# Kernel tuning notes

Hardware: AMD Instinct MI355X
Metric: run time of the kernel (lower is better)

## Reference

```python
import jax, jax.numpy as jnp
import numpy as np

MIN_NORM = 1e-15
EPS = 1e-5
C_CURV = 1.0  # args.c

def _norm(x):
    return jnp.clip(jnp.linalg.norm(x, axis=-1, keepdims=True), MIN_NORM)

def artanh(x):
    x = jnp.clip(x, -1.0 + EPS, 1.0 - EPS)
    return 0.5 * (jnp.log1p(x) - jnp.log1p(-x))

def proj(x, c):
    # clip points to stay strictly inside the Poincare ball
    norm = _norm(x)
    maxnorm = (1.0 - EPS) / jnp.sqrt(c)
    return jnp.where(norm > maxnorm, x / norm * maxnorm, x)

def expmap0(u, c):
    sqrt_c = jnp.sqrt(c)
    u_norm = _norm(u)
    return jnp.tanh(sqrt_c * u_norm) * u / (sqrt_c * u_norm)

def logmap0(p, c):
    sqrt_c = jnp.sqrt(c)
    p_norm = _norm(p)
    return artanh(sqrt_c * p_norm) * p / (sqrt_c * p_norm)

def mobius_add(x, y, c):
    x2 = jnp.sum(x * x, axis=-1, keepdims=True)
    y2 = jnp.sum(y * y, axis=-1, keepdims=True)
    xy = jnp.sum(x * y, axis=-1, keepdims=True)
    num = (1.0 + 2.0 * c * xy + c * y2) * x + (1.0 - c * x2) * y
    denom = 1.0 + 2.0 * c * xy + c * c * x2 * y2
    return num / jnp.clip(denom, MIN_NORM)

def mobius_matvec(W, x, c):
    sqrt_c = jnp.sqrt(c)
    x_norm = _norm(x)
    mx = x @ W.T
    mx_norm = _norm(mx)
    return jnp.tanh(mx_norm / x_norm * artanh(sqrt_c * x_norm)) * mx / (mx_norm * sqrt_c)

def poincare_dist(x, y, c):
    sqrt_c = jnp.sqrt(c)
    d = _norm(mobius_add(-x, y, c))[..., 0]
    return 2.0 / sqrt_c * artanh(sqrt_c * d)

def hgnn_layer(h, adj, W, b, c):
    # HypLinear: mobius matvec + hyperbolic bias
    mv = proj(mobius_matvec(W, h, c), c)
    hyp_b = proj(expmap0(b, c), c)
    h = proj(mobius_add(mv, hyp_b, c), c)
    # HypAgg: aggregate in tangent space at origin
    h = proj(expmap0(adj @ logmap0(h, c), c), c)
    # HypAct: relu in tangent space
    return proj(expmap0(jax.nn.relu(logmap0(h, c)), c), c)

def setup_inputs() -> dict:
    key = jax.random.key(0)
    ks = jax.random.split(key, 10)
    N, D, C, NC, NODE_C, L = 8192, 128, 64, 7, 7, 4
    x = jax.random.normal(ks[0], (N, D), jnp.float32)
    adj = jax.random.uniform(ks[1], (N, N), jnp.float32) / N  # row-stochastic-ish dense adjacency
    graph_indicator = jax.random.randint(ks[2], (N,), 0, 1)
    W_conv = jax.random.normal(ks[3], (L, D, D), jnp.float32) / np.sqrt(D)
    b_conv = jax.random.normal(ks[4], (L, D), jnp.float32) * 0.01
    centroids = jax.random.normal(ks[5], (C, D), jnp.float32) * 0.1
    W_mlp = jax.random.normal(ks[6], (NC, C), jnp.float32) * 0.1
    b_mlp = jnp.zeros((NC,), jnp.float32)
    W_mlp1 = jax.random.normal(ks[7], (NODE_C, D), jnp.float32) * 0.1
    b_mlp1 = jnp.zeros((NODE_C,), jnp.float32)
    return {"x": x, "adj": adj, "graph_indicator": graph_indicator,
            "W_conv": W_conv, "b_conv": b_conv, "centroids": centroids,
            "W_mlp": W_mlp, "b_mlp": b_mlp, "W_mlp1": W_mlp1, "b_mlp1": b_mlp1}

def reference(x, adj, graph_indicator, W_conv, b_conv, centroids, W_mlp, b_mlp, W_mlp1, b_mlp1):
    c = C_CURV
    # proj_tan0 is identity for PoincareBall
    h = proj(expmap0(x, c), c)
    # 2 residual blocks, each with 2 HGNN layers; shortcut is identity (in_dim == out_dim)
    for blk in range(2):
        res = h
        for j in range(2):
            idx = blk * 2 + j
            h = hgnn_layer(h, adj, W_conv[idx], b_conv[idx], c)
        h = h + res  # Euclidean residual, as in the source
    # CentroidDistance: pairwise hyperbolic distance [N, C]
    node_centroid_dist = poincare_dist(h[:, None, :], centroids[None, :, :], c)
    readout = jnp.mean(node_centroid_dist, axis=0, keepdims=True)  # [1, C]
    h_r = logmap0(readout, c)  # proj_tan0(logmap0(.)) -> identity proj_tan0
    logits = jax.nn.softmax(h_r @ W_mlp.T + b_mlp, axis=0)[None]        # [1,1,NC]
    h1 = logmap0(h, c)
    logits_node = jax.nn.softmax(h1 @ W_mlp1.T + b_mlp1, axis=0)[None]  # [1,N,node_classes]
    return (logits, logits_node, h_r)
```

## Files before the change

### kernel.cpp

```cpp
#include <hip/hip_runtime.h>

#define MIN_NORM 1e-15f
#define EPSV 1e-5f
#define MAXN (1.0f - EPSV)
#define NN 8192
#define DD 128

typedef unsigned short u16;
typedef __bf16 bf16x8 __attribute__((ext_vector_type(8)));
typedef float f32x4 __attribute__((ext_vector_type(4)));

__device__ __forceinline__ float wave_sum(float v) {
#pragma unroll
  for (int off = 32; off > 0; off >>= 1) v += __shfl_xor(v, off, 64);
  return v;
}

__device__ __forceinline__ float artanh_f(float x) {
  x = fminf(fmaxf(x, -1.0f + EPSV), 1.0f - EPSV);
  return 0.5f * (log1pf(x) - log1pf(-x));
}

__device__ __forceinline__ u16 f2bf(float f) {
  unsigned u = __float_as_uint(f);
  unsigned r = (u + 0x7fffu + ((u >> 16) & 1u)) >> 16;
  return (u16)r;
}
__device__ __forceinline__ float bf2f(u16 b) { return __uint_as_float(((unsigned)b) << 16); }

__device__ __forceinline__ void gload16(const u16* g, u16* l) {
  __builtin_amdgcn_global_load_lds((const __attribute__((address_space(1))) void*)(g),
                                   (__attribute__((address_space(3))) void*)(l), 16, 0, 0);
}

template <bool TILED>
__global__ __launch_bounds__(256) void gemm_bt(const u16* __restrict__ A,
                                               const u16* __restrict__ Bt,
                                               float* __restrict__ Cp,
                                               int M, int K, int KC) {
  __shared__ __align__(16) u16 Ash[3 * 64 * 64];
  __shared__ __align__(16) u16 Bsh[3 * 128 * 64];

  const int tid = threadIdx.x;
  const int lane = tid & 63;
  const int w = tid >> 6;
  const int wm = w >> 1, wn = w & 1;
  const int lrow = lane & 15;
  const int lq = lane >> 4;
  const int m0 = blockIdx.x * 64;
  const int kk0 = blockIdx.y * KC;
  const int kt0 = kk0 >> 6;
  const int bxK = blockIdx.x * (K >> 6);

  const int srow = lane >> 3;
  const int spc = lane & 7;

  const u16* Ap = A + (TILED ? 0 : (size_t)m0 * K);

  f32x4 acc[2][4];
#pragma unroll
  for (int a = 0; a < 2; a++)
#pragma unroll
    for (int b = 0; b < 4; b++)
#pragma unroll
      for (int r = 0; r < 4; r++) acc[a][b][r] = 0.0f;

#define STAGE(bf, tkt, kk)                                                     \
  do {                                                                         \
    if constexpr (TILED) {                                                     \
      const u16* at = A + (((size_t)(bxK + (tkt))) << 12) + (lane << 3);       \
      _Pragma("unroll") for (int ii = 0; ii < 2; ii++)                         \
        gload16(at + ((ii * 4 + w) << 9), &Ash[(bf) * 4096 + ((ii * 4 + w) << 9)]); \
      const u16* bt2 = Bt + (((size_t)(tkt)) << 13) + (lane << 3);             \
      _Pragma("unroll") for (int ii = 0; ii < 4; ii++)                         \
        gload16(bt2 + ((ii * 4 + w) << 9), &Bsh[(bf) * 8192 + ((ii * 4 + w) << 9)]); \
    } else {                                                                   \
      _Pragma("unroll") for (int ii = 0; ii < 2; ii++) {                       \
        int rw = ((ii * 4 + w) << 3) + srow;                                   \
        gload16(Ap + (size_t)rw * K + (kk) + ((spc ^ (rw & 7)) << 3),          \
                &Ash[(bf) * 4096 + ((ii * 4 + w) << 9)]);                      \
      }                                                                        \
      _Pragma("unroll") for (int ii = 0; ii < 4; ii++) {                       \
        int rw = ((ii * 4 + w) << 3) + srow;                                   \
        gload16(Bt + (size_t)rw * K + (kk) + ((spc ^ (rw & 7)) << 3),          \
                &Bsh[(bf) * 8192 + ((ii * 4 + w) << 9)]);                      \
      }                                                                        \
    }                                                                          \
  } while (0)

#define COMPUTE(bf)                                                            \
  do {                                                                         \
    const int abase = (bf) * 4096, bbase = (bf) * 8192;                        \
    _Pragma("unroll") for (int ks = 0; ks < 2; ks++) {                         \
      const int lc = ks * 4 + lq;                                              \
      bf16x8 af[2], bfr[4];                                                    \
      _Pragma("unroll") for (int ti = 0; ti < 2; ti++) {                       \
        int r = wm * 32 + ti * 16 + lrow;                                      \
        af[ti] = *(const bf16x8*)&Ash[abase + r * 64 + ((lc ^ (r & 7)) << 3)]; \
      }                                                                        \
      _Pragma("unroll") for (int tj = 0; tj < 4; tj++) {                       \
        int n = wn * 64 + tj * 16 + lrow;                                      \
        bfr[tj] = *(const bf16x8*)&Bsh[bbase + n * 64 + ((lc ^ (n & 7)) << 3)]; \
      }                                                                        \
      _Pragma("unroll") for (int ti = 0; ti < 2; ti++)                         \
        _Pragma("unroll") for (int tj = 0; tj < 4; tj++)                       \
          acc[ti][tj] = __builtin_amdgcn_mfma_f32_16x16x32_bf16(af[ti], bfr[tj], acc[ti][tj], 0, 0, 0); \
    }                                                                          \
  } while (0)

  const int nt = KC >> 6;
  STAGE(0, kt0, kk0);
  if (nt > 1) STAGE(1, kt0 + 1, kk0 + 64);

  for (int t = 0; t < nt - 1; t++) {
    asm volatile("s_waitcnt vmcnt(6)" ::: "memory");
    __builtin_amdgcn_s_barrier();
    if (t + 2 < nt) {
      const int b2 = (t + 2) % 3;
      STAGE(b2, kt0 + t + 2, kk0 + (t + 2) * 64);
    }
    COMPUTE(t % 3);
  }
  asm volatile("s_waitcnt vmcnt(0)" ::: "memory");
  __builtin_amdgcn_s_barrier();
  COMPUTE((nt - 1) % 3);
#undef STAGE
#undef COMPUTE

  float* C = Cp + (size_t)blockIdx.y * M * 128;
#pragma unroll
  for (int ti = 0; ti < 2; ti++)
#pragma unroll
    for (int tj = 0; tj < 4; tj++)
#pragma unroll
      for (int r = 0; r < 4; r++) {
        int row = m0 + wm * 32 + ti * 16 + lq * 4 + r;
        int col = wn * 64 + tj * 16 + lrow;
        C[(size_t)row * 128 + col] = acc[ti][tj][r];
      }
}

__global__ __launch_bounds__(256) void cvt_tile(const float* __restrict__ src,
                                                u16* __restrict__ dst) {
  int tid = threadIdx.x;
  int xb = blockIdx.x;
  int kg = blockIdx.y;
  int ch = tid & 63;
  int rs = tid >> 6;
#pragma unroll
  for (int rr = 0; rr < 16; rr++) {
    int row = rr * 4 + rs;
    int gk = kg * 512 + ch * 8;
    const float* s = src + (size_t)(xb * 64 + row) * NN + gk;
    float4 a = *(const float4*)s;
    float4 b = *(const float4*)(s + 4);
    ushort4 d0, d1;
    d0.x = f2bf(a.x); d0.y = f2bf(a.y); d0.z = f2bf(a.z); d0.w = f2bf(a.w);
    d1.x = f2bf(b.x); d1.y = f2bf(b.y); d1.z = f2bf(b.z); d1.w = f2bf(b.w);
    u16* d = dst + (((size_t)(xb * 128 + (gk >> 6))) << 12) + row * 64 +
             ((((gk >> 3) & 7) ^ (row & 7)) << 3);
    *(ushort4*)d = d0;
    *(ushort4*)(d + 4) = d1;
  }
}

__global__ void build_wt(const float* __restrict__ W, u16* __restrict__ Wt2) {
  int idx = blockIdx.x * 256 + threadIdx.x;
  if (idx >= 4 * 128 * 128) return;
  int layer = idx >> 14;
  int n = (idx >> 7) & 127;
  int k = idx & 127;
  float e = W[idx];
  u16 hi = f2bf(e);
  u16 lo = f2bf(e - bf2f(hi));
  u16* base = Wt2 + (size_t)layer * 128 * 384 + (size_t)n * 384;
  base[k] = hi;
  base[128 + k] = hi;
  base[256 + k] = lo;
}

__device__ __forceinline__ void write_split(u16* hs, int i, int lane, float v0, float v1) {
  u16* row = hs + (size_t)i * 384;
  u16 h0 = f2bf(v0), h1 = f2bf(v1);
  u16 l0 = f2bf(v0 - bf2f(h0)), l1 = f2bf(v1 - bf2f(h1));
  row[lane] = h0;         row[lane + 64] = h1;
  row[128 + lane] = l0;   row[128 + 64 + lane] = l1;
  row[256 + lane] = h0;   row[256 + 64 + lane] = h1;
}

__global__ __launch_bounds__(64) void rowwise_init(const float* __restrict__ x,
                                                   float* __restrict__ h,
                                                   float* __restrict__ res,
                                                   u16* __restrict__ hsplit) {
  int i = blockIdx.x, lane = threadIdx.x;
  const float* xr = x + (size_t)i * DD;
  float a0 = xr[lane], a1 = xr[lane + 64];
  float n = fmaxf(sqrtf(wave_sum(a0 * a0 + a1 * a1)), MIN_NORM);
  float g = tanhf(n) / n;
  float y0 = g * a0, y1 = g * a1;
  float pn = fmaxf(sqrtf(wave_sum(y0 * y0 + y1 * y1)), MIN_NORM);
  float s = pn > MAXN ? MAXN / pn : 1.0f;
  y0 *= s; y1 *= s;
  size_t base = (size_t)i * DD;
  h[base + lane] = y0;   h[base + lane + 64] = y1;
  res[base + lane] = y0; res[base + lane + 64] = y1;
  write_split(hsplit, i, lane, y0, y1);
}

__global__ __launch_bounds__(64) void rowwise_mid(const float* __restrict__ h,
                                                  const float* __restrict__ P,
                                                  const float* __restrict__ bvec,
                                                  u16* __restrict__ uT2) {
  int i = blockIdx.x, lane = threadIdx.x;
  size_t base = (size_t)i * DD;
  const float* hr = h + base;
  float h0 = hr[lane], h1 = hr[lane + 64];
  float m0 = 0.f, m1 = 0.f;
#pragma unroll
  for (int sk = 0; sk < 3; sk++) {
    const float* p = P + (size_t)sk * NN * DD + base;
    m0 += p[lane];
    m1 += p[lane + 64];
  }
  float xn = fmaxf(sqrtf(wave_sum(h0 * h0 + h1 * h1)), MIN_NORM);
  float mn = fmaxf(sqrtf(wave_sum(m0 * m0 + m1 * m1)), MIN_NORM);
  float t = tanhf(mn / xn * artanh_f(xn));
  float v0 = t * m0 / mn, v1 = t * m1 / mn;
  float pn = fmaxf(sqrtf(wave_sum(v0 * v0 + v1 * v1)), MIN_NORM);
  float sc = pn > MAXN ? MAXN / pn : 1.0f;
  v0 *= sc; v1 *= sc;
  float b0 = bvec[lane], b1 = bvec[lane + 64];
  float bn = fmaxf(sqrtf(wave_sum(b0 * b0 + b1 * b1)), MIN_NORM);
  float gb = tanhf(bn) / bn;
  float e0 = gb * b0, e1 = gb * b1;
  float en = fmaxf(sqrtf(wave_sum(e0 * e0 + e1 * e1)), MIN_NORM);
  float sb = en > MAXN ? MAXN / en : 1.0f;
  e0 *= sb; e1 *= sb;
  float x2 = wave_sum(v0 * v0 + v1 * v1);
  float y2 = wave_sum(e0 * e0 + e1 * e1);
  float xy = wave_sum(v0 * e0 + v1 * e1);
  float ca = 1.0f + 2.0f * xy + y2;
  float cb = 1.0f - x2;
  float den = fmaxf(1.0f + 2.0f * xy + x2 * y2, MIN_NORM);
  float t0 = (ca * v0 + cb * e0) / den, t1 = (ca * v1 + cb * e1) / den;
  float tn = fmaxf(sqrtf(wave_sum(t0 * t0 + t1 * t1)), MIN_NORM);
  float st = tn > MAXN ? MAXN / tn : 1.0f;
  t0 *= st; t1 *= st;
  float pn2 = fmaxf(sqrtf(wave_sum(t0 * t0 + t1 * t1)), MIN_NORM);
  float gl = artanh_f(pn2) / pn2;
  u16* tb = uT2 + (((size_t)(i >> 6)) << 13);
  int c8 = (i >> 3) & 7, k7 = i & 7;
  tb[lane * 64 + (((c8) ^ (lane & 7)) << 3) + k7] = f2bf(gl * t0);
  int n2 = lane + 64;
  tb[n2 * 64 + (((c8) ^ (n2 & 7)) << 3) + k7] = f2bf(gl * t1);
}

__global__ __launch_bounds__(64) void rowwise_post(const float* __restrict__ P,
                                                   float* __restrict__ h,
                                                   float* __restrict__ res,
                                                   u16* __restrict__ hsplit,
                                                   int addres) {
  int i = blockIdx.x, lane = threadIdx.x;
  size_t base = (size_t)i * DD;
  float m0 = 0.f, m1 = 0.f;
#pragma unroll
  for (int sk = 0; sk < 8; sk++) {
    const float* p = P + (size_t)sk * NN * DD + base;
    m0 += p[lane];
    m1 += p[lane + 64];
  }
  float n = fmaxf(sqrtf(wave_sum(m0 * m0 + m1 * m1)), MIN_NORM);
  float g = tanhf(n) / n;
  float y0 = g * m0, y1 = g * m1;
  float pn = fmaxf(sqrtf(wave_sum(y0 * y0 + y1 * y1)), MIN_NORM);
  float s = pn > MAXN ? MAXN / pn : 1.0f;
  y0 *= s; y1 *= s;
  float hn = fmaxf(sqrtf(wave_sum(y0 * y0 + y1 * y1)), MIN_NORM);
  float gl = artanh_f(hn) / hn;
  float u0 = fmaxf(gl * y0, 0.0f), u1 = fmaxf(gl * y1, 0.0f);
  float un = fmaxf(sqrtf(wave_sum(u0 * u0 + u1 * u1)), MIN_NORM);
  float ge = tanhf(un) / un;
  float z0 = ge * u0, z1 = ge * u1;
  float zn = fmaxf(sqrtf(wave_sum(z0 * z0 + z1 * z1)), MIN_NORM);
  float sz = zn > MAXN ? MAXN / zn : 1.0f;
  z0 *= sz; z1 *= sz;
  if (addres) {
    z0 += res[base + lane];
    z1 += res[base + lane + 64];
    res[base + lane] = z0;
    res[base + lane + 64] = z1;
  }
  h[base + lane] = z0;
  h[base + lane + 64] = z1;
  write_split(hsplit, i, lane, z0, z1);
}

__global__ __launch_bounds__(256) void centroid_k(const float* __restrict__ h,
                                                  const float* __restrict__ cen,
                                                  float* __restrict__ rs) {
  __shared__ float cs[64 * 129];
  __shared__ float hs[32 * 128];
  __shared__ float y2s[64];
  int tid = threadIdx.x;
  int i0 = blockIdx.x * 32;
  for (int idx = tid; idx < 64 * 128; idx += 256) {
    int r = idx >> 7, c = idx & 127;
    cs[r * 129 + c] = cen[idx];
  }
  for (int idx = tid; idx < 32 * 128; idx += 256) hs[idx] = h[(size_t)i0 * 128 + idx];
  __syncthreads();
  if (tid < 64) {
    float s = 0.f;
    for (int k = 0; k < 128; k++) { float v = cs[tid * 129 + k]; s = fmaf(v, v, s); }
    y2s[tid] = s;
  }
  __syncthreads();
  int w = tid >> 6, lane = tid & 63;
  float dsum = 0.f;
  for (int rr = 0; rr < 8; rr++) {
    int r = w * 8 + rr;
    float dot = 0.f, x2 = 0.f;
    for (int k = 0; k < 128; k++) {
      float hk = hs[r * 128 + k];
      dot = fmaf(hk, cs[lane * 129 + k], dot);
      x2 = fmaf(hk, hk, x2);
    }
    float y2 = y2s[lane];
    float al = 1.0f - 2.0f * dot + y2;
    float be = 1.0f - x2;
    float num2 = al * al * x2 + be * be * y2 - 2.0f * al * be * dot;
    float den = fmaxf(1.0f - 2.0f * dot + x2 * y2, MIN_NORM);
    float d = fmaxf(sqrtf(fmaxf(num2, 0.0f)) / den, MIN_NORM);
    dsum += 2.0f * artanh_f(d);
  }
  atomicAdd(&rs[lane], dsum);
}

__global__ __launch_bounds__(64) void finalize_k(const float* __restrict__ rs,
                                                 float* __restrict__ out) {
  int lane = threadIdx.x;
  float r = rs[lane] * (1.0f / 8192.0f);
  float n = fmaxf(sqrtf(wave_sum(r * r)), MIN_NORM);
  float a = artanh_f(n);
  out[7 + NN * 7 + lane] = a * r / n;
  if (lane < 7) out[lane] = 1.0f;
}

__global__ __launch_bounds__(64) void scores_k(const float* __restrict__ h,
                                               const float* __restrict__ Wm,
                                               const float* __restrict__ bm,
                                               float* __restrict__ sc) {
  int i = blockIdx.x, lane = threadIdx.x;
  const float* hr = h + (size_t)i * DD;
  float h0 = hr[lane], h1 = hr[lane + 64];
  float pn = fmaxf(sqrtf(wave_sum(h0 * h0 + h1 * h1)), MIN_NORM);
  float gl = artanh_f(pn) / pn;
  float u0 = gl * h0, u1 = gl * h1;
  float p[7];
#pragma unroll
  for (int j = 0; j < 7; j++)
    p[j] = wave_sum(u0 * Wm[j * 128 + lane] + u1 * Wm[j * 128 + lane + 64]);
  float v = p[0];
#pragma unroll
  for (int j = 1; j < 7; j++)
    if (lane == j) v = p[j];
  if (lane < 7) sc[(size_t)i * 7 + lane] = v + bm[lane];
}

__global__ __launch_bounds__(256) void softmax_col(const float* __restrict__ sc,
                                                   float* __restrict__ out) {
  __shared__ float buf[256][8];
  int tid = threadIdx.x;
  float mx[7];
#pragma unroll
  for (int j = 0; j < 7; j++) mx[j] = -1e30f;
  for (int i = tid; i < NN; i += 256)
#pragma unroll
    for (int j = 0; j < 7; j++) mx[j] = fmaxf(mx[j], sc[i * 7 + j]);
#pragma unroll
  for (int j = 0; j < 7; j++) buf[tid][j] = mx[j];
  __syncthreads();
  for (int off = 128; off > 0; off >>= 1) {
    if (tid < off)
#pragma unroll
      for (int j = 0; j < 7; j++) buf[tid][j] = fmaxf(buf[tid][j], buf[tid + off][j]);
    __syncthreads();
  }
  float cm[7];
#pragma unroll
  for (int j = 0; j < 7; j++) cm[j] = buf[0][j];
  __syncthreads();
  float sm[7];
#pragma unroll
  for (int j = 0; j < 7; j++) sm[j] = 0.f;
  for (int i = tid; i < NN; i += 256)
#pragma unroll
    for (int j = 0; j < 7; j++) sm[j] += expf(sc[i * 7 + j] - cm[j]);
#pragma unroll
  for (int j = 0; j < 7; j++) buf[tid][j] = sm[j];
  __syncthreads();
  for (int off = 128; off > 0; off >>= 1) {
    if (tid < off)
#pragma unroll
      for (int j = 0; j < 7; j++) buf[tid][j] += buf[tid + off][j];
    __syncthreads();
  }
  float csum[7];
#pragma unroll
  for (int j = 0; j < 7; j++) csum[j] = buf[0][j];
  __syncthreads();
  for (int idx = tid; idx < NN * 7; idx += 256) {
    int i = idx / 7, j = idx - i * 7;
    out[idx] = expf(sc[i * 7 + j] - cm[j]) / csum[j];
  }
}

extern "C" void kernel_launch(void* const* d_in, const int* in_sizes, int n_in,
                              void* d_out, int out_size, void* d_ws, size_t ws_size,
                              hipStream_t stream) {
  const float* x = (const float*)d_in[0];
  const float* adj = (const float*)d_in[1];
  const float* W_conv = (const float*)d_in[3];
  const float* b_conv = (const float*)d_in[4];
  const float* centroids = (const float*)d_in[5];
  const float* W_mlp1 = (const float*)d_in[8];
  const float* b_mlp1 = (const float*)d_in[9];
  float* out = (float*)d_out;

  char* ws = (char*)d_ws;
  size_t off = 0;
  auto alloc = [&](size_t bytes) {
    void* p = ws + off;
    off = (off + bytes + 255) & ~(size_t)255;
    return p;
  };
  float* h = (float*)alloc((size_t)NN * DD * 4);
  float* res = (float*)alloc((size_t)NN * DD * 4);
  u16* hsplit = (u16*)alloc((size_t)NN * 384 * 2);
  u16* uT2 = (u16*)alloc((size_t)DD * NN * 2);
  u16* Wt2 = (u16*)alloc((size_t)4 * 128 * 384 * 2);
  float* P = (float*)alloc((size_t)8 * NN * DD * 4);
  u16* adjT = (u16*)alloc((size_t)NN * NN * 2);
  float* scores = (float*)alloc((size_t)NN * 7 * 4);
  float* rs = (float*)alloc(64 * 4);
  (void)ws_size; (void)in_sizes; (void)n_in; (void)out_size;

  hipMemsetAsync(rs, 0, 64 * 4, stream);
  build_wt<<<(4 * 128 * 128 + 255) / 256, 256, 0, stream>>>(W_conv, Wt2);
  rowwise_init<<<NN, 64, 0, stream>>>(x, h, res, hsplit);
  cvt_tile<<<dim3(128, 16), 256, 0, stream>>>(adj, adjT);
  for (int layer = 0; layer < 4; layer++) {
    gemm_bt<false><<<dim3(NN / 64, 3), 256, 0, stream>>>(
        hsplit, Wt2 + (size_t)layer * 128 * 384, P, NN, 384, 128);
    rowwise_mid<<<NN, 64, 0, stream>>>(h, P, b_conv + layer * DD, uT2);
    gemm_bt<true><<<dim3(NN / 64, 8), 256, 0, stream>>>(
        adjT, uT2, P, NN, NN, NN / 8);
    rowwise_post<<<NN, 64, 0, stream>>>(P, h, res, hsplit, (layer & 1));
  }
  centroid_k<<<256, 256, 0, stream>>>(h, centroids, rs);
  finalize_k<<<1, 64, 0, stream>>>(rs, out);
  scores_k<<<NN, 64, 0, stream>>>(h, W_mlp1, b_mlp1, scores);
  softmax_col<<<1, 256, 0, stream>>>(scores, out + 7);
}
```

Measured before the change: 812.5 us.

## Fuse HypLinear epilogue into W GEMM, parallelize column softmax, halve adj split-K

Drops the split-K W GEMM plus separate rowwise_mid kernel. A single GEMM over full K now computes per-row norms and the bias dot product through shuffle and LDS reductions, then applies the Mobius/proj/logmap math in its epilogue and writes the tiled bf16 operand directly. Bias expmap/proj and the input row norms are precomputed in small kernels. The adj GEMM split-K goes from 8 to 4, which cuts partial-sum traffic but leaves fewer blocks. The single-block column softmax is replaced by atomicMax with an order-preserving encoding, a multi-block sum with atomicAdd, and a parallel write kernel.

```diff
diff --git a/kernel.cpp b/kernel.cpp
--- a/kernel.cpp
+++ b/kernel.cpp
@@ -28,16 +28,24 @@
 }
 __device__ __forceinline__ float bf2f(u16 b) { return __uint_as_float(((unsigned)b) << 16); }
 
+__device__ __forceinline__ unsigned fenc(float x) {
+  unsigned u = __float_as_uint(x);
+  return (u & 0x80000000u) ? ~u : (u | 0x80000000u);
+}
+__device__ __forceinline__ float fdec(unsigned k) {
+  unsigned u = (k & 0x80000000u) ? (k & 0x7fffffffu) : ~k;
+  return __uint_as_float(u);
+}
+
 __device__ __forceinline__ void gload16(const u16* g, u16* l) {
   __builtin_amdgcn_global_load_lds((const __attribute__((address_space(1))) void*)(g),
                                    (__attribute__((address_space(3))) void*)(l), 16, 0, 0);
 }
 
-template <bool TILED>
-__global__ __launch_bounds__(256) void gemm_bt(const u16* __restrict__ A,
-                                               const u16* __restrict__ Bt,
-                                               float* __restrict__ Cp,
-                                               int M, int K, int KC) {
+__global__ __launch_bounds__(256) void gemm_adj(const u16* __restrict__ A,
+                                                const u16* __restrict__ Bt,
+                                                float* __restrict__ Cp,
+                                                int KC) {
   __shared__ __align__(16) u16 Ash[3 * 64 * 64];
   __shared__ __align__(16) u16 Bsh[3 * 128 * 64];
 
@@ -48,14 +56,8 @@
   const int lrow = lane & 15;
   const int lq = lane >> 4;
   const int m0 = blockIdx.x * 64;
-  const int kk0 = blockIdx.y * KC;
-  const int kt0 = kk0 >> 6;
-  const int bxK = blockIdx.x * (K >> 6);
-
-  const int srow = lane >> 3;
-  const int spc = lane & 7;
-
-  const u16* Ap = A + (TILED ? 0 : (size_t)m0 * K);
+  const int kt0 = (blockIdx.y * KC) >> 6;
+  const int bxK = blockIdx.x * (NN >> 6);
 
   f32x4 acc[2][4];
 #pragma unroll
@@ -65,60 +67,43 @@
 #pragma unroll
       for (int r = 0; r < 4; r++) acc[a][b][r] = 0.0f;
 
-#define STAGE(bf, tkt, kk)                                                     \
-  do {                                                                         \
-    if constexpr (TILED) {                                                     \
-      const u16* at = A + (((size_t)(bxK + (tkt))) << 12) + (lane << 3);       \
-      _Pragma("unroll") for (int ii = 0; ii < 2; ii++)                         \
-        gload16(at + ((ii * 4 + w) << 9), &Ash[(bf) * 4096 + ((ii * 4 + w) << 9)]); \
-      const u16* bt2 = Bt + (((size_t)(tkt)) << 13) + (lane << 3);             \
-      _Pragma("unroll") for (int ii = 0; ii < 4; ii++)                         \
-        gload16(bt2 + ((ii * 4 + w) << 9), &Bsh[(bf) * 8192 + ((ii * 4 + w) << 9)]); \
-    } else {                                                                   \
-      _Pragma("unroll") for (int ii = 0; ii < 2; ii++) {                       \
-        int rw = ((ii * 4 + w) << 3) + srow;                                   \
-        gload16(Ap + (size_t)rw * K + (kk) + ((spc ^ (rw & 7)) << 3),          \
-                &Ash[(bf) * 4096 + ((ii * 4 + w) << 9)]);                      \
-      }                                                                        \
-      _Pragma("unroll") for (int ii = 0; ii < 4; ii++) {                       \
-        int rw = ((ii * 4 + w) << 3) + srow;                                   \
-        gload16(Bt + (size_t)rw * K + (kk) + ((spc ^ (rw & 7)) << 3),          \
-                &Bsh[(bf) * 8192 + ((ii * 4 + w) << 9)]);                      \
-      }                                                                        \
-    }                                                                          \
+#define STAGE(bf, tkt)                                                          \
+  do {                                                                          \
+    const u16* at = A + (((size_t)(bxK + (tkt))) << 12) + (lane << 3);          \
+    _Pragma("unroll") for (int ii = 0; ii < 2; ii++)                            \
+      gload16(at + ((ii * 4 + w) << 9), &Ash[(bf) * 4096 + ((ii * 4 + w) << 9)]); \
+    const u16* bt2 = Bt + (((size_t)(tkt)) << 13) + (lane << 3);                \
+    _Pragma("unroll") for (int ii = 0; ii < 4; ii++)                            \
+      gload16(bt2 + ((ii * 4 + w) << 9), &Bsh[(bf) * 8192 + ((ii * 4 + w) << 9)]); \
   } while (0)
 
-#define COMPUTE(bf)                                                            \
-  do {                                                                         \
-    const int abase = (bf) * 4096, bbase = (bf) * 8192;                        \
-    _Pragma("unroll") for (int ks = 0; ks < 2; ks++) {                         \
-      const int lc = ks * 4 + lq;                                              \
-      bf16x8 af[2], bfr[4];                                                    \
-      _Pragma("unroll") for (int ti = 0; ti < 2; ti++) {                       \
-        int r = wm * 32 + ti * 16 + lrow;                                      \
-        af[ti] = *(const bf16x8*)&Ash[abase + r * 64 + ((lc ^ (r & 7)) << 3)]; \
-      }                                                                        \
-      _Pragma("unroll") for (int tj = 0; tj < 4; tj++) {                       \
-        int n = wn * 64 + tj * 16 + lrow;                                      \
+#define COMPUTE(bf)                                                             \
+  do {                                                                          \
+    const int abase = (bf) * 4096, bbase = (bf) * 8192;                         \
+    _Pragma("unroll") for (int ks = 0; ks < 2; ks++) {                          \
+      const int lc = ks * 4 + lq;                                               \
+      bf16x8 af[2], bfr[4];                                                     \
+      _Pragma("unroll") for (int ti = 0; ti < 2; ti++) {                        \
+        int r = wm * 32 + ti * 16 + lrow;                                       \
+        af[ti] = *(const bf16x8*)&Ash[abase + r * 64 + ((lc ^ (r & 7)) << 3)];  \
+      }                                                                         \
+      _Pragma("unroll") for (int tj = 0; tj < 4; tj++) {                        \
+        int n = wn * 64 + tj * 16 + lrow;                                       \
         bfr[tj] = *(const bf16x8*)&Bsh[bbase + n * 64 + ((lc ^ (n & 7)) << 3)]; \
-      }                                                                        \
-      _Pragma("unroll") for (int ti = 0; ti < 2; ti++)                         \
-        _Pragma("unroll") for (int tj = 0; tj < 4; tj++)                       \
+      }                                                                         \
+      _Pragma("unroll") for (int ti = 0; ti < 2; ti++)                          \
+        _Pragma("unroll") for (int tj = 0; tj < 4; tj++)                        \
           acc[ti][tj] = __builtin_amdgcn_mfma_f32_16x16x32_bf16(af[ti], bfr[tj], acc[ti][tj], 0, 0, 0); \
-    }                                                                          \
+    }                                                                           \
   } while (0)
 
   const int nt = KC >> 6;
-  STAGE(0, kt0, kk0);
-  if (nt > 1) STAGE(1, kt0 + 1, kk0 + 64);
-
+  STAGE(0, kt0);
+  STAGE(1, kt0 + 1);
   for (int t = 0; t < nt - 1; t++) {
     asm volatile("s_waitcnt vmcnt(6)" ::: "memory");
     __builtin_amdgcn_s_barrier();
-    if (t + 2 < nt) {
-      const int b2 = (t + 2) % 3;
-      STAGE(b2, kt0 + t + 2, kk0 + (t + 2) * 64);
-    }
+    if (t + 2 < nt) STAGE((t + 2) % 3, kt0 + t + 2);
     COMPUTE(t % 3);
   }
   asm volatile("s_waitcnt vmcnt(0)" ::: "memory");
@@ -127,7 +112,7 @@
 #undef STAGE
 #undef COMPUTE
 
-  float* C = Cp + (size_t)blockIdx.y * M * 128;
+  float* C = Cp + (size_t)blockIdx.y * NN * 128;
 #pragma unroll
   for (int ti = 0; ti < 2; ti++)
 #pragma unroll
@@ -138,6 +123,150 @@
         int col = wn * 64 + tj * 16 + lrow;
         C[(size_t)row * 128 + col] = acc[ti][tj][r];
       }
+}
+
+__global__ __launch_bounds__(256) void wgemm_mid(const u16* __restrict__ A,
+                                                 const u16* __restrict__ Bt,
+                                                 const float* __restrict__ hnorm,
+                                                 const float* __restrict__ eb,
+                                                 const float* __restrict__ ey2,
+                                                 u16* __restrict__ uT2) {
+  __shared__ __align__(16) u16 Ash[3 * 64 * 64];
+  __shared__ __align__(16) u16 Bsh[3 * 128 * 64];
+
+  const int tid = threadIdx.x;
+  const int lane = tid & 63;
+  const int w = tid >> 6;
+  const int wm = w >> 1, wn = w & 1;
+  const int lrow = lane & 15;
+  const int lq = lane >> 4;
+  const int m0 = blockIdx.x * 64;
+  const int srow = lane >> 3, spc = lane & 7;
+  const int K = 384;
+  const u16* Ap = A + (size_t)m0 * K;
+
+  f32x4 acc[2][4];
+#pragma unroll
+  for (int a = 0; a < 2; a++)
+#pragma unroll
+    for (int b = 0; b < 4; b++)
+#pragma unroll
+      for (int r = 0; r < 4; r++) acc[a][b][r] = 0.0f;
+
+#define STAGE(bf, kk)                                                           \
+  do {                                                                          \
+    _Pragma("unroll") for (int ii = 0; ii < 2; ii++) {                          \
+      int rw = ((ii * 4 + w) << 3) + srow;                                      \
+      gload16(Ap + (size_t)rw * K + (kk) + ((spc ^ (rw & 7)) << 3),             \
+              &Ash[(bf) * 4096 + ((ii * 4 + w) << 9)]);                         \
+    }                                                                           \
+    _Pragma("unroll") for (int ii = 0; ii < 4; ii++) {                          \
+      int rw = ((ii * 4 + w) << 3) + srow;                                      \
+      gload16(Bt + (size_t)rw * K + (kk) + ((spc ^ (rw & 7)) << 3),             \
+              &Bsh[(bf) * 8192 + ((ii * 4 + w) << 9)]);                         \
+    }                                                                           \
+  } while (0)
+
+#define COMPUTE(bf)                                                             \
+  do {                                                                          \
+    const int abase = (bf) * 4096, bbase = (bf) * 8192;                         \
+    _Pragma("unroll") for (int ks = 0; ks < 2; ks++) {                          \
+      const int lc = ks * 4 + lq;                                               \
+      bf16x8 af[2], bfr[4];                                                     \
+      _Pragma("unroll") for (int ti = 0; ti < 2; ti++) {                        \
+        int r = wm * 32 + ti * 16 + lrow;                                       \
+        af[ti] = *(const bf16x8*)&Ash[abase + r * 64 + ((lc ^ (r & 7)) << 3)];  \
+      }                                                                         \
+      _Pragma("unroll") for (int tj = 0; tj < 4; tj++) {                        \
+        int n = wn * 64 + tj * 16 + lrow;                                       \
+        bfr[tj] = *(const bf16x8*)&Bsh[bbase + n * 64 + ((lc ^ (n & 7)) << 3)]; \
+      }                                                                         \
+      _Pragma("unroll") for (int ti = 0; ti < 2; ti++)                          \
+        _Pragma("unroll") for (int tj = 0; tj < 4; tj++)                        \
+          acc[ti][tj] = __builtin_amdgcn_mfma_f32_16x16x32_bf16(af[ti], bfr[tj], acc[ti][tj], 0, 0, 0); \
+    }                                                                           \
+  } while (0)
+
+  const int nt = 6;
+  STAGE(0, 0);
+  STAGE(1, 64);
+  for (int t = 0; t < nt - 1; t++) {
+    asm volatile("s_waitcnt vmcnt(6)" ::: "memory");
+    __builtin_amdgcn_s_barrier();
+    if (t + 2 < nt) STAGE((t + 2) % 3, (t + 2) * 64);
+    COMPUTE(t % 3);
+  }
+  asm volatile("s_waitcnt vmcnt(0)" ::: "memory");
+  __builtin_amdgcn_s_barrier();
+  COMPUTE((nt - 1) % 3);
+#undef STAGE
+#undef COMPUTE
+
+  float ecol[4];
+#pragma unroll
+  for (int tj = 0; tj < 4; tj++) ecol[tj] = eb[wn * 64 + tj * 16 + lrow];
+
+  float* sred = (float*)Ash;
+#pragma unroll
+  for (int ti = 0; ti < 2; ti++)
+#pragma unroll
+    for (int r = 0; r < 4; r++) {
+      float p2 = 0.f, pe = 0.f;
+#pragma unroll
+      for (int tj = 0; tj < 4; tj++) {
+        float v = acc[ti][tj][r];
+        p2 = fmaf(v, v, p2);
+        pe = fmaf(v, ecol[tj], pe);
+      }
+#pragma unroll
+      for (int off = 1; off < 16; off <<= 1) {
+        p2 += __shfl_xor(p2, off, 64);
+        pe += __shfl_xor(pe, off, 64);
+      }
+      if (lrow == 0) {
+        int row = wm * 32 + ti * 16 + lq * 4 + r;
+        sred[row * 4 + wn * 2 + 0] = p2;
+        sred[row * 4 + wn * 2 + 1] = pe;
+      }
+    }
+  __syncthreads();
+
+  const float y2v = *ey2;
+  u16* tb = uT2 + ((size_t)blockIdx.x << 13);
+#pragma unroll
+  for (int ti = 0; ti < 2; ti++)
+#pragma unroll
+    for (int r = 0; r < 4; r++) {
+      int row = wm * 32 + ti * 16 + lq * 4 + r;
+      float s2 = sred[row * 4 + 0] + sred[row * 4 + 2];
+      float se = sred[row * 4 + 1] + sred[row * 4 + 3];
+      float xn = hnorm[m0 + row];
+      float mn = fmaxf(sqrtf(s2), MIN_NORM);
+      float t = tanhf(mn / xn * artanh_f(xn));
+      float vs = t / mn;
+      float pn = fmaxf(sqrtf(vs * vs * s2), MIN_NORM);
+      float sc2 = pn > MAXN ? MAXN / pn : 1.0f;
+      float al = vs * sc2;
+      float x2 = al * al * s2;
+      float xy = al * se;
+      float ca = 1.0f + 2.0f * xy + y2v;
+      float cb = 1.0f - x2;
+      float den = fmaxf(1.0f + 2.0f * xy + x2 * y2v, MIN_NORM);
+      float tn2 = ca * ca * x2 + 2.0f * ca * cb * xy + cb * cb * y2v;
+      float tn = fmaxf(sqrtf(fmaxf(tn2, 0.0f)) / den, MIN_NORM);
+      float st = tn > MAXN ? MAXN / tn : 1.0f;
+      float pn2 = fmaxf(tn * st, MIN_NORM);
+      float gl = artanh_f(pn2) / pn2;
+      float Ar = gl * st * ca * al / den;
+      float Br = gl * st * cb / den;
+      int c8 = (row >> 3) & 7, k7 = row & 7;
+#pragma unroll
+      for (int tj = 0; tj < 4; tj++) {
+        int n = wn * 64 + tj * 16 + lrow;
+        float u = Ar * acc[ti][tj][r] + Br * ecol[tj];
+        tb[n * 64 + ((c8 ^ (n & 7)) << 3) + k7] = f2bf(u);
+      }
+    }
 }
 
 __global__ __launch_bounds__(256) void cvt_tile(const float* __restrict__ src,
@@ -179,6 +308,24 @@
   base[256 + k] = lo;
 }
 
+__global__ __launch_bounds__(64) void prep_bias(const float* __restrict__ bconv,
+                                                float* __restrict__ ebuf,
+                                                float* __restrict__ ey2) {
+  int layer = blockIdx.x, lane = threadIdx.x;
+  const float* bvec = bconv + layer * DD;
+  float b0 = bvec[lane], b1 = bvec[lane + 64];
+  float bn = fmaxf(sqrtf(wave_sum(b0 * b0 + b1 * b1)), MIN_NORM);
+  float gb = tanhf(bn) / bn;
+  float e0 = gb * b0, e1 = gb * b1;
+  float en = fmaxf(sqrtf(wave_sum(e0 * e0 + e1 * e1)), MIN_NORM);
+  float sb = en > MAXN ? MAXN / en : 1.0f;
+  e0 *= sb; e1 *= sb;
+  float y2 = wave_sum(e0 * e0 + e1 * e1);
+  ebuf[layer * DD + lane] = e0;
+  ebuf[layer * DD + lane + 64] = e1;
+  if (lane == 0) ey2[layer] = y2;
+}
+
 __device__ __forceinline__ void write_split(u16* hs, int i, int lane, float v0, float v1) {
   u16* row = hs + (size_t)i * 384;
   u16 h0 = f2bf(v0), h1 = f2bf(v1);
@@ -191,7 +338,8 @@
 __global__ __launch_bounds__(64) void rowwise_init(const float* __restrict__ x,
                                                    float* __restrict__ h,
                                                    float* __restrict__ res,
-                                                   u16* __restrict__ hsplit) {
+                                                   u16* __restrict__ hsplit,
+                                                   float* __restrict__ hnorm) {
   int i = blockIdx.x, lane = threadIdx.x;
   const float* xr = x + (size_t)i * DD;
   float a0 = xr[lane], a1 = xr[lane + 64];
@@ -205,66 +353,21 @@
   h[base + lane] = y0;   h[base + lane + 64] = y1;
   res[base + lane] = y0; res[base + lane + 64] = y1;
   write_split(hsplit, i, lane, y0, y1);
-}
-
-__global__ __launch_bounds__(64) void rowwise_mid(const float* __restrict__ h,
-                                                  const float* __restrict__ P,
-                                                  const float* __restrict__ bvec,
-                                                  u16* __restrict__ uT2) {
-  int i = blockIdx.x, lane = threadIdx.x;
-  size_t base = (size_t)i * DD;
-  const float* hr = h + base;
-  float h0 = hr[lane], h1 = hr[lane + 64];
-  float m0 = 0.f, m1 = 0.f;
-#pragma unroll
-  for (int sk = 0; sk < 3; sk++) {
-    const float* p = P + (size_t)sk * NN * DD + base;
-    m0 += p[lane];
-    m1 += p[lane + 64];
-  }
-  float xn = fmaxf(sqrtf(wave_sum(h0 * h0 + h1 * h1)), MIN_NORM);
-  float mn = fmaxf(sqrtf(wave_sum(m0 * m0 + m1 * m1)), MIN_NORM);
-  float t = tanhf(mn / xn * artanh_f(xn));
-  float v0 = t * m0 / mn, v1 = t * m1 / mn;
-  float pn = fmaxf(sqrtf(wave_sum(v0 * v0 + v1 * v1)), MIN_NORM);
-  float sc = pn > MAXN ? MAXN / pn : 1.0f;
-  v0 *= sc; v1 *= sc;
-  float b0 = bvec[lane], b1 = bvec[lane + 64];
-  float bn = fmaxf(sqrtf(wave_sum(b0 * b0 + b1 * b1)), MIN_NORM);
-  float gb = tanhf(bn) / bn;
-  float e0 = gb * b0, e1 = gb * b1;
-  float en = fmaxf(sqrtf(wave_sum(e0 * e0 + e1 * e1)), MIN_NORM);
-  float sb = en > MAXN ? MAXN / en : 1.0f;
-  e0 *= sb; e1 *= sb;
-  float x2 = wave_sum(v0 * v0 + v1 * v1);
-  float y2 = wave_sum(e0 * e0 + e1 * e1);
-  float xy = wave_sum(v0 * e0 + v1 * e1);
-  float ca = 1.0f + 2.0f * xy + y2;
-  float cb = 1.0f - x2;
-  float den = fmaxf(1.0f + 2.0f * xy + x2 * y2, MIN_NORM);
-  float t0 = (ca * v0 + cb * e0) / den, t1 = (ca * v1 + cb * e1) / den;
-  float tn = fmaxf(sqrtf(wave_sum(t0 * t0 + t1 * t1)), MIN_NORM);
-  float st = tn > MAXN ? MAXN / tn : 1.0f;
-  t0 *= st; t1 *= st;
-  float pn2 = fmaxf(sqrtf(wave_sum(t0 * t0 + t1 * t1)), MIN_NORM);
-  float gl = artanh_f(pn2) / pn2;
-  u16* tb = uT2 + (((size_t)(i >> 6)) << 13);
-  int c8 = (i >> 3) & 7, k7 = i & 7;
-  tb[lane * 64 + (((c8) ^ (lane & 7)) << 3) + k7] = f2bf(gl * t0);
-  int n2 = lane + 64;
-  tb[n2 * 64 + (((c8) ^ (n2 & 7)) << 3) + k7] = f2bf(gl * t1);
+  float hn = fmaxf(sqrtf(wave_sum(y0 * y0 + y1 * y1)), MIN_NORM);
+  if (lane == 0) hnorm[i] = hn;
 }
 
 __global__ __launch_bounds__(64) void rowwise_post(const float* __restrict__ P,
                                                    float* __restrict__ h,
                                                    float* __restrict__ res,
                                                    u16* __restrict__ hsplit,
+                                                   float* __restrict__ hnorm,
                                                    int addres) {
   int i = blockIdx.x, lane = threadIdx.x;
   size_t base = (size_t)i * DD;
   float m0 = 0.f, m1 = 0.f;
 #pragma unroll
-  for (int sk = 0; sk < 8; sk++) {
+  for (int sk = 0; sk < 4; sk++) {
     const float* p = P + (size_t)sk * NN * DD + base;
     m0 += p[lane];
     m1 += p[lane + 64];
@@ -293,6 +396,8 @@
   h[base + lane] = z0;
   h[base + lane + 64] = z1;
   write_split(hsplit, i, lane, z0, z1);
+  float hn2 = fmaxf(sqrtf(wave_sum(z0 * z0 + z1 * z1)), MIN_NORM);
+  if (lane == 0) hnorm[i] = hn2;
 }
 
 __global__ __launch_bounds__(256) void centroid_k(const float* __restrict__ h,
@@ -349,7 +454,8 @@
 __global__ __launch_bounds__(64) void scores_k(const float* __restrict__ h,
                                                const float* __restrict__ Wm,
                                                const float* __restrict__ bm,
-                                               float* __restrict__ sc) {
+                                               float* __restrict__ sc,
+                                               unsigned* __restrict__ cmaxU) {
   int i = blockIdx.x, lane = threadIdx.x;
   const float* hr = h + (size_t)i * DD;
   float h0 = hr[lane], h1 = hr[lane + 64];
@@ -364,55 +470,43 @@
 #pragma unroll
   for (int j = 1; j < 7; j++)
     if (lane == j) v = p[j];
-  if (lane < 7) sc[(size_t)i * 7 + lane] = v + bm[lane];
-}
-
-__global__ __launch_bounds__(256) void softmax_col(const float* __restrict__ sc,
-                                                   float* __restrict__ out) {
+  if (lane < 7) {
+    float sv = v + bm[lane];
+    sc[(size_t)i * 7 + lane] = sv;
+    atomicMax(&cmaxU[lane], fenc(sv));
+  }
+}
+
+__global__ __launch_bounds__(256) void sm_sum(const float* __restrict__ sc,
+                                              const unsigned* __restrict__ cmaxU,
+                                              float* __restrict__ csum) {
   __shared__ float buf[256][8];
   int tid = threadIdx.x;
-  float mx[7];
-#pragma unroll
-  for (int j = 0; j < 7; j++) mx[j] = -1e30f;
-  for (int i = tid; i < NN; i += 256)
-#pragma unroll
-    for (int j = 0; j < 7; j++) mx[j] = fmaxf(mx[j], sc[i * 7 + j]);
-#pragma unroll
-  for (int j = 0; j < 7; j++) buf[tid][j] = mx[j];
+  int i = blockIdx.x * 256 + tid;
+  float cm[7];
+#pragma unroll
+  for (int j = 0; j < 7; j++) cm[j] = fdec(cmaxU[j]);
+#pragma unroll
+  for (int j = 0; j < 7; j++) buf[tid][j] = expf(sc[i * 7 + j] - cm[j]);
   __syncthreads();
   for (int off = 128; off > 0; off >>= 1) {
     if (tid < off)
 #pragma unroll
-      for (int j = 0; j < 7; j++) buf[tid][j] = fmaxf(buf[tid][j], buf[tid + off][j]);
-    __syncthreads();
-  }
-  float cm[7];
-#pragma unroll
-  for (int j = 0; j < 7; j++) cm[j] = buf[0][j];
-  __syncthreads();
-  float sm[7];
-#pragma unroll
-  for (int j = 0; j < 7; j++) sm[j] = 0.f;
-  for (int i = tid; i < NN; i += 256)
-#pragma unroll
-    for (int j = 0; j < 7; j++) sm[j] += expf(sc[i * 7 + j] - cm[j]);
-#pragma unroll
-  for (int j = 0; j < 7; j++) buf[tid][j] = sm[j];
-  __syncthreads();
-  for (int off = 128; off > 0; off >>= 1) {
-    if (tid < off)
-#pragma unroll
       for (int j = 0; j < 7; j++) buf[tid][j] += buf[tid + off][j];
     __syncthreads();
   }
-  float csum[7];
-#pragma unroll
-  for (int j = 0; j < 7; j++) csum[j] = buf[0][j];
-  __syncthreads();
-  for (int idx = tid; idx < NN * 7; idx += 256) {
-    int i = idx / 7, j = idx - i * 7;
-    out[idx] = expf(sc[i * 7 + j] - cm[j]) / csum[j];
-  }
+  if (tid < 7) atomicAdd(&csum[tid], buf[0][tid]);
+}
+
+__global__ __launch_bounds__(256) void sm_write(const float* __restrict__ sc,
+                                                const unsigned* __restrict__ cmaxU,
+                                                const float* __restrict__ csum,
+                                                float* __restrict__ out) {
+  int idx = blockIdx.x * 256 + threadIdx.x;
+  if (idx >= NN * 7) return;
+  int i = idx / 7, j = idx - i * 7;
+  float cm = fdec(cmaxU[j]);
+  out[idx] = expf(sc[i * 7 + j] - cm) / csum[j];
 }
 
 extern "C" void kernel_launch(void* const* d_in, const int* in_sizes, int n_in,
@@ -439,26 +533,32 @@
   u16* hsplit = (u16*)alloc((size_t)NN * 384 * 2);
   u16* uT2 = (u16*)alloc((size_t)DD * NN * 2);
   u16* Wt2 = (u16*)alloc((size_t)4 * 128 * 384 * 2);
-  float* P = (float*)alloc((size_t)8 * NN * DD * 4);
+  float* P = (float*)alloc((size_t)4 * NN * DD * 4);
   u16* adjT = (u16*)alloc((size_t)NN * NN * 2);
   float* scores = (float*)alloc((size_t)NN * 7 * 4);
-  float* rs = (float*)alloc(64 * 4);
+  float* hnorm = (float*)alloc((size_t)NN * 4);
+  float* ebuf = (float*)alloc(4 * DD * 4);
+  float* ey2 = (float*)alloc(4 * 4);
+  float* zblk = (float*)alloc(768);
+  float* rs = zblk;
+  unsigned* cmaxU = (unsigned*)(zblk + 64);
+  float* csum = zblk + 72;
   (void)ws_size; (void)in_sizes; (void)n_in; (void)out_size;
 
-  hipMemsetAsync(rs, 0, 64 * 4, stream);
+  hipMemsetAsync(zblk, 0, 768, stream);
   build_wt<<<(4 * 128 * 128 + 255) / 256, 256, 0, stream>>>(W_conv, Wt2);
-  rowwise_init<<<NN, 64, 0, stream>>>(x, h, res, hsplit);
+  prep_bias<<<4, 64, 0, stream>>>(b_conv, ebuf, ey2);
+  rowwise_init<<<NN, 64, 0, stream>>>(x, h, res, hsplit, hnorm);
   cvt_tile<<<dim3(128, 16), 256, 0, stream>>>(adj, adjT);
   for (int layer = 0; layer < 4; layer++) {
-    gemm_bt<false><<<dim3(NN / 64, 3), 256, 0, stream>>>(
-        hsplit, Wt2 + (size_t)layer * 128 * 384, P, NN, 384, 128);
-    rowwise_mid<<<NN, 64, 0, stream>>>(h, P, b_conv + layer * DD, uT2);
-    gemm_bt<true><<<dim3(NN / 64, 8), 256, 0, stream>>>(
-        adjT, uT2, P, NN, NN, NN / 8);
-    rowwise_post<<<NN, 64, 0, stream>>>(P, h, res, hsplit, (layer & 1));
+    wgemm_mid<<<NN / 64, 256, 0, stream>>>(hsplit, Wt2 + (size_t)layer * 128 * 384,
+                                           hnorm, ebuf + layer * DD, ey2 + layer, uT2);
+    gemm_adj<<<dim3(NN / 64, 4), 256, 0, stream>>>(adjT, uT2, P, NN / 4);
+    rowwise_post<<<NN, 64, 0, stream>>>(P, h, res, hsplit, hnorm, (layer & 1));
   }
   centroid_k<<<256, 256, 0, stream>>>(h, centroids, rs);
   finalize_k<<<1, 64, 0, stream>>>(rs, out);
-  scores_k<<<NN, 64, 0, stream>>>(h, W_mlp1, b_mlp1, scores);
-  softmax_col<<<1, 256, 0, stream>>>(scores, out + 7);
-}
+  scores_k<<<NN, 64, 0, stream>>>(h, W_mlp1, b_mlp1, scores, cmaxU);
+  sm_sum<<<NN / 256, 256, 0, stream>>>(scores, cmaxU, csum);
+  sm_write<<<(NN * 7 + 255) / 256, 256, 0, stream>>>(scores, cmaxU, csum, out + 7);
+}
```

Result: no change. 814.6 us (+0.3%).
